# Optimization experiments

Measured on AMD Instinct MI355X. Metric: run time of the kernel, lower is better.

## Reference

```python
import jax, jax.numpy as jnp
import numpy as np

N = 50000; E = 150000
NODE_IN = 16; EDGE_IN = 19; H = 32  # H = max(2*node_in, 32)
LEAK = 0.1; EPS = 1e-5
LAYER_DINS = (16, 32, 32)


def _leaky(x):
    return jnp.where(x >= 0, x, LEAK * x)


def _bn(x, g, b):
    # BatchNorm1d in training mode: batch statistics, biased variance
    m = x.mean(0)
    v = x.var(0)
    return (x - m) * jax.lax.rsqrt(v + EPS) * g + b


def setup_inputs() -> dict:
    key = jax.random.key(0)
    keys = iter(jax.random.split(key, 64))

    def rn(shape, s=0.05):
        return jax.random.normal(next(keys), shape, dtype=jnp.float32) * s

    inp = {
        'x': jax.random.normal(next(keys), (N, NODE_IN), dtype=jnp.float32),
        'edge_index': jax.random.randint(next(keys), (2, E), 0, N),
        'e': jax.random.normal(next(keys), (E, EDGE_IN), dtype=jnp.float32),
        'xbatch': jnp.zeros((N,), dtype=jnp.int32),
        'bn_node_g': jnp.ones((NODE_IN,), jnp.float32), 'bn_node_b': jnp.zeros((NODE_IN,), jnp.float32),
        'bn_edge_g': jnp.ones((EDGE_IN,), jnp.float32), 'bn_edge_b': jnp.zeros((EDGE_IN,), jnp.float32),
    }
    for l, din in enumerate(LAYER_DINS):
        inp[f'l{l}_nnW1'] = rn((EDGE_IN, din));      inp[f'l{l}_nnb1'] = jnp.zeros((din,), jnp.float32)
        inp[f'l{l}_nnW2'] = rn((din, din * H));       inp[f'l{l}_nnb2'] = jnp.zeros((din * H,), jnp.float32)
        inp[f'l{l}_root'] = rn((din, H));             inp[f'l{l}_bias'] = jnp.zeros((H,), jnp.float32)
    # MetaLayer predictor: EdgeModel(H, EDGE_IN, leak) and NodeModel(H, 2, leak)
    inp['em_W1'] = rn((2 * H + EDGE_IN, H)); inp['em_b1'] = jnp.zeros((H,), jnp.float32)
    inp['em_W2'] = rn((H, H));               inp['em_b2'] = jnp.zeros((H,), jnp.float32)
    inp['nm1_W1'] = rn((2 * H, H));          inp['nm1_b1'] = jnp.zeros((H,), jnp.float32)
    inp['nm1_W2'] = rn((H, H));              inp['nm1_b2'] = jnp.zeros((H,), jnp.float32)
    inp['nm2_W1'] = rn((2 * H, H));          inp['nm2_b1'] = jnp.zeros((H,), jnp.float32)
    inp['nm2_W2'] = rn((H, 2));              inp['nm2_b2'] = jnp.zeros((2,), jnp.float32)
    return inp


def _forward(x, e, edge_index, p):
    (bn_node_g, bn_node_b, bn_edge_g, bn_edge_b,
     l0_nnW1, l0_nnb1, l0_nnW2, l0_nnb2, l0_root, l0_bias,
     l1_nnW1, l1_nnb1, l1_nnW2, l1_nnb2, l1_root, l1_bias,
     l2_nnW1, l2_nnb1, l2_nnW2, l2_nnb2, l2_root, l2_bias,
     em_W1, em_b1, em_W2, em_b2,
     nm1_W1, nm1_b1, nm1_W2, nm1_b2,
     nm2_W1, nm2_b1, nm2_W2, nm2_b2) = p

    e = _bn(e, bn_edge_g, bn_edge_b)
    x = _bn(x, bn_node_g, bn_node_b)
    row, col = edge_index[0], edge_index[1]  # source, target (PyG convention)

    layers = [(l0_nnW1, l0_nnb1, l0_nnW2, l0_nnb2, l0_root, l0_bias),
              (l1_nnW1, l1_nnb1, l1_nnW2, l1_nnb2, l1_root, l1_bias),
              (l2_nnW1, l2_nnb1, l2_nnW2, l2_nnb2, l2_root, l2_bias)]
    for (W1, b1, W2, b2, root, bias), din in zip(layers, LAYER_DINS):
        # edge MLP -> per-edge weight matrix [E, din, H]
        w = _leaky(_leaky(e @ W1 + b1) @ W2 + b2).reshape(E, din, H)
        msg = jnp.einsum('ei,eio->eo', x[row], w)              # gather + per-edge matvec
        agg = jax.ops.segment_sum(msg, col, num_segments=N)     # scatter-add ('add' aggr)
        x = agg + x @ root + bias                                # NNConv root weight + bias

    # MetaLayer predictor
    e2 = _leaky(jnp.concatenate([x[row], x[col], e], axis=1) @ em_W1 + em_b1) @ em_W2 + em_b2
    h = _leaky(jnp.concatenate([x[row], e2], axis=1) @ nm1_W1 + nm1_b1) @ nm1_W2 + nm1_b2
    cnt = jnp.clip(jax.ops.segment_sum(jnp.ones((E,), x.dtype), col, num_segments=N), 1.0)
    agg = jax.ops.segment_sum(h, col, num_segments=N) / cnt[:, None]
    xo = _leaky(jnp.concatenate([x, agg], axis=1) @ nm2_W1 + nm2_b1) @ nm2_W2 + nm2_b2
    return jax.nn.log_softmax(xo, axis=1)  # [N, 2] node_pred


def reference(x, edge_index, e, xbatch,
              bn_node_g, bn_node_b, bn_edge_g, bn_edge_b,
              l0_nnW1, l0_nnb1, l0_nnW2, l0_nnb2, l0_root, l0_bias,
              l1_nnW1, l1_nnb1, l1_nnW2, l1_nnb2, l1_root, l1_bias,
              l2_nnW1, l2_nnb1, l2_nnW2, l2_nnb2, l2_root, l2_bias,
              em_W1, em_b1, em_W2, em_b2,
              nm1_W1, nm1_b1, nm1_W2, nm1_b2,
              nm2_W1, nm2_b1, nm2_W2, nm2_b2):
    p = (bn_node_g, bn_node_b, bn_edge_g, bn_edge_b,
         l0_nnW1, l0_nnb1, l0_nnW2, l0_nnb2, l0_root, l0_bias,
         l1_nnW1, l1_nnb1, l1_nnW2, l1_nnb2, l1_root, l1_bias,
         l2_nnW1, l2_nnb1, l2_nnW2, l2_nnb2, l2_root, l2_bias,
         em_W1, em_b1, em_W2, em_b2,
         nm1_W1, nm1_b1, nm1_W2, nm1_b2,
         nm2_W1, nm2_b1, nm2_W2, nm2_b2)
    return _forward(x, e, edge_index, p)
```

## Files before the change

kernel.cpp:

```cpp
#include <hip/hip_runtime.h>
#include <math.h>

constexpr int NN  = 50000;
constexpr int NE  = 150000;
constexpr int NIN = 16;
constexpr int EIN = 19;
constexpr int HD  = 32;
constexpr int NTILES = NE / 16;
constexpr int NBLK_E = 128;
constexpr int NBLK_X = 64;

#define LEAK  0.1f
#define BNEPS 1e-5f

typedef __attribute__((ext_vector_type(8))) short bfrag;
typedef __attribute__((ext_vector_type(4))) float f32x4;
typedef __attribute__((ext_vector_type(2))) float f32x2;
typedef __attribute__((ext_vector_type(4))) int   i32x4;

__device__ __forceinline__ float lky(float v){ return fmaxf(v, LEAK*v); }
__device__ __forceinline__ unsigned f2bf(float f){
  unsigned u = __float_as_uint(f);
  return ((u + 0x7FFFu + ((u >> 16) & 1u)) >> 16);
}
__device__ __forceinline__ void split8(const float* v, i32x4& h4, i32x4& l4){
  unsigned hs[8], ls[8];
  #pragma unroll
  for(int j = 0; j < 8; j++){
    unsigned hh = f2bf(v[j]);
    float hf = __uint_as_float(hh << 16);
    hs[j] = hh; ls[j] = f2bf(v[j] - hf);
  }
  h4[0] = (int)(hs[0] | (hs[1]<<16)); h4[1] = (int)(hs[2] | (hs[3]<<16));
  h4[2] = (int)(hs[4] | (hs[5]<<16)); h4[3] = (int)(hs[6] | (hs[7]<<16));
  l4[0] = (int)(ls[0] | (ls[1]<<16)); l4[1] = (int)(ls[2] | (ls[3]<<16));
  l4[2] = (int)(ls[4] | (ls[5]<<16)); l4[3] = (int)(ls[6] | (ls[7]<<16));
}

__global__ void zero_kernel(float* __restrict__ p, int n){
  int stride = gridDim.x * blockDim.x;
  for(int i = blockIdx.x*blockDim.x + threadIdx.x; i < n; i += stride) p[i] = 0.f;
}

__global__ __launch_bounds__(256) void stats_all_kernel(const float* __restrict__ e,
                                                        const float* __restrict__ x,
                                                        float* __restrict__ partial_e,
                                                        float* __restrict__ partial_x){
  __shared__ float red[4][40];
  const int tid = threadIdx.x, lane = tid & 63, wid = tid >> 6;
  if(blockIdx.x < NBLK_E){
    float s[EIN], q[EIN];
    #pragma unroll
    for(int c = 0; c < EIN; c++){ s[c] = 0.f; q[c] = 0.f; }
    const int gstride = NBLK_E * 256;
    for(int g = blockIdx.x*256 + tid; g < NE/4; g += gstride){
      const f32x4* p = (const f32x4*)(e + (size_t)g * 76);
      #pragma unroll
      for(int m = 0; m < 19; m++){
        f32x4 v = p[m];
        #pragma unroll
        for(int j = 0; j < 4; j++){
          int c = (4*m + j) % 19;
          s[c] += v[j]; q[c] = fmaf(v[j], v[j], q[c]);
        }
      }
    }
    #pragma unroll
    for(int off = 32; off; off >>= 1){
      #pragma unroll
      for(int c = 0; c < EIN; c++){ s[c] += __shfl_xor(s[c], off); q[c] += __shfl_xor(q[c], off); }
    }
    if(lane == 0){
      #pragma unroll
      for(int c = 0; c < EIN; c++){ red[wid][c] = s[c]; red[wid][20 + c] = q[c]; }
    }
    __syncthreads();
    if(tid < 39 && tid != 19)
      partial_e[blockIdx.x*40 + tid] = red[0][tid] + red[1][tid] + red[2][tid] + red[3][tid];
  } else {
    float s[NIN], q[NIN];
    #pragma unroll
    for(int c = 0; c < NIN; c++){ s[c] = 0.f; q[c] = 0.f; }
    const int bid = blockIdx.x - NBLK_E;
    const int gstride = NBLK_X * 256;
    for(int r = bid*256 + tid; r < NN; r += gstride){
      const f32x4* p = (const f32x4*)(x + (size_t)r * NIN);
      #pragma unroll
      for(int m = 0; m < 4; m++){
        f32x4 v = p[m];
        #pragma unroll
        for(int j = 0; j < 4; j++){
          int c = 4*m + j;
          s[c] += v[j]; q[c] = fmaf(v[j], v[j], q[c]);
        }
      }
    }
    #pragma unroll
    for(int off = 32; off; off >>= 1){
      #pragma unroll
      for(int c = 0; c < NIN; c++){ s[c] += __shfl_xor(s[c], off); q[c] += __shfl_xor(q[c], off); }
    }
    if(lane == 0){
      #pragma unroll
      for(int c = 0; c < NIN; c++){ red[wid][c] = s[c]; red[wid][16 + c] = q[c]; }
    }
    __syncthreads();
    if(tid < 32)
      partial_x[bid*32 + tid] = red[0][tid] + red[1][tid] + red[2][tid] + red[3][tid];
  }
}

__global__ __launch_bounds__(1024) void prep_kernel(const float* __restrict__ partial_e,
                                                    const float* __restrict__ partial_x,
                                                    const float* __restrict__ ge, const float* __restrict__ be,
                                                    const float* __restrict__ gx, const float* __restrict__ bx,
                                                    const float* __restrict__ l0W1, const float* __restrict__ l0b1,
                                                    const float* __restrict__ l1W1, const float* __restrict__ l1b1,
                                                    const float* __restrict__ l2W1, const float* __restrict__ l2b1,
                                                    const float* __restrict__ emW1, const float* __restrict__ emb1,
                                                    const float* __restrict__ emW2, const float* __restrict__ emb2,
                                                    const float* __restrict__ nm1W1, const float* __restrict__ nm1b1,
                                                    const float* __restrict__ nm1W2, const float* __restrict__ nm1b2,
                                                    float* __restrict__ ss_g, float* __restrict__ W1f,
                                                    float* __restrict__ b1f, float* __restrict__ biasP,
                                                    short* __restrict__ predpk){
  __shared__ float ss[70];
  __shared__ float emW1f[608];
  __shared__ float emb1f[32];
  __shared__ float predW[7168];
  const int t = threadIdx.x;

  if(t < EIN){
    float s = 0.f, q = 0.f;
    for(int b = 0; b < NBLK_E; b++){ s += partial_e[b*40 + t]; q += partial_e[b*40 + 20 + t]; }
    float m = s / (float)NE;
    float v = q / (float)NE - m*m;
    float sc = ge[t] * rsqrtf(v + BNEPS);
    ss[t] = sc; ss[EIN + t] = be[t] - m*sc;
  } else if(t >= 32 && t < 32 + NIN){
    int c = t - 32;
    float s = 0.f, q = 0.f;
    for(int b = 0; b < NBLK_X; b++){ s += partial_x[b*32 + c]; q += partial_x[b*32 + 16 + c]; }
    float m = s / (float)NN;
    float v = q / (float)NN - m*m;
    float sc = gx[c] * rsqrtf(v + BNEPS);
    ss[2*EIN + c] = sc; ss[2*EIN + NIN + c] = bx[c] - m*sc;
  }
  __syncthreads();
  if(t < 70) ss_g[t] = ss[t];

  if(t < 128){
    int seg = t >> 5, j = t & 31;
    if(seg == 0){
      if(j < NIN){
        float acc = l0b1[j];
        for(int k = 0; k < EIN; k++){
          W1f[0*640 + k*NIN + j] = ss[k] * l0W1[k*NIN + j];
          acc += ss[EIN+k] * l0W1[k*NIN + j];
        }
        b1f[0*32 + j] = acc;
      }
    } else if(seg == 1){
      float acc = l1b1[j];
      for(int k = 0; k < EIN; k++){
        W1f[1*640 + k*HD + j] = ss[k] * l1W1[k*HD + j];
        acc += ss[EIN+k] * l1W1[k*HD + j];
      }
      b1f[1*32 + j] = acc;
    } else if(seg == 2){
      float acc = l2b1[j];
      for(int k = 0; k < EIN; k++){
        W1f[2*640 + k*HD + j] = ss[k] * l2W1[k*HD + j];
        acc += ss[EIN+k] * l2W1[k*HD + j];
      }
      b1f[2*32 + j] = acc;
    } else {
      float acc = emb1[j];
      for(int k = 0; k < EIN; k++){
        emW1f[k*HD + j] = ss[k] * emW1[(2*HD+k)*HD + j];
        acc += ss[EIN+k] * emW1[(2*HD+k)*HD + j];
      }
      emb1f[j] = acc;
    }
  }
  __syncthreads();

  for(int i = t; i < 224*32; i += 1024){
    int k = i >> 5, n = i & 31;
    float v;
    if(k < 64)       v = emW1[k*32 + n];
    else if(k < 83)  v = emW1f[(k-64)*32 + n];
    else if(k < 96)  v = 0.f;
    else if(k < 128) v = emW2[(k-96)*32 + n];
    else if(k < 192) v = nm1W1[(k-128)*32 + n];
    else             v = nm1W2[(k-192)*32 + n];
    predW[i] = v;
  }
  if(t < 128){
    int s = t >> 5, n = t & 31;
    biasP[t] = (s==0) ? emb1f[n] : (s==1) ? emb2[n] : (s==2) ? nm1b1[n] : nm1b2[n];
  }
  __syncthreads();

  for(int idx = t; idx < 14*512; idx += 1024){
    int c = idx >> 9, l = (idx >> 3) & 63, j = idx & 7;
    int kbg = c >> 1, nc = c & 1;
    int k = kbg*32 + 8*(l>>4) + j;
    int n = nc*16 + (l & 15);
    predpk[idx] = (short)f2bf(predW[k*32 + n]);
  }
}

__global__ __launch_bounds__(256) void w2pack_all_kernel(const float* __restrict__ W20,
                                                         const float* __restrict__ W21,
                                                         const float* __restrict__ W22,
                                                         short* __restrict__ w2pk){
  int idx = blockIdx.x*256 + threadIdx.x;
  if(idx >= 81920) return;
  const float* W2; int DIN, base, ci;
  if(idx < 16384){ W2 = W20; DIN = 16; base = 0;     ci = idx; }
  else if(idx < 49152){ W2 = W21; DIN = 32; base = 32768; ci = idx - 16384; }
  else { W2 = W22; DIN = 32; base = 65536; ci = idx - 49152; }
  int c = ci >> 9, l = (ci >> 3) & 63, j = ci & 7;
  int k = 8*(l>>4) + j;
  int n = c*16 + (l & 15);
  float v = (k < DIN) ? W2[(size_t)k*(DIN*HD) + n] : 0.f;
  w2pk[base + ci] = (short)f2bf(v);
}

__global__ __launch_bounds__(256) void rootn_kernel(const float* __restrict__ x,
                                                    const float* __restrict__ ssx,
                                                    const float* __restrict__ root,
                                                    const float* __restrict__ bias,
                                                    float* __restrict__ x_a){
  __shared__ float rs[NIN*HD];
  __shared__ float scs[NIN], shs[NIN], bs[HD];
  const int tid = threadIdx.x;
  for(int i = tid; i < NIN*HD; i += 256) rs[i] = root[i];
  if(tid < NIN){ scs[tid] = ssx[tid]; shs[tid] = ssx[NIN + tid]; }
  else if(tid < NIN + HD) bs[tid - NIN] = bias[tid - NIN];
  __syncthreads();

  int n = blockIdx.x*256 + tid;
  if(n >= NN) return;
  float xb[NIN];
  const f32x4* xp = (const f32x4*)(x + (size_t)n*NIN);
  #pragma unroll
  for(int g = 0; g < 4; g++){
    f32x4 v = xp[g];
    #pragma unroll
    for(int j = 0; j < 4; j++) xb[g*4+j] = fmaf(v[j], scs[g*4+j], shs[g*4+j]);
  }
  f32x4 a0 = *(const f32x4*)&bs[0],  a1 = *(const f32x4*)&bs[4];
  f32x4 a2 = *(const f32x4*)&bs[8],  a3 = *(const f32x4*)&bs[12];
  f32x4 a4 = *(const f32x4*)&bs[16], a5 = *(const f32x4*)&bs[20];
  f32x4 a6 = *(const f32x4*)&bs[24], a7 = *(const f32x4*)&bs[28];
  #pragma unroll
  for(int k = 0; k < NIN; k++){
    float v = xb[k];
    const f32x4* wp = (const f32x4*)&rs[k*HD];
    f32x4 vv = {v,v,v,v};
    a0 = __builtin_elementwise_fma(vv, wp[0], a0);
    a1 = __builtin_elementwise_fma(vv, wp[1], a1);
    a2 = __builtin_elementwise_fma(vv, wp[2], a2);
    a3 = __builtin_elementwise_fma(vv, wp[3], a3);
    a4 = __builtin_elementwise_fma(vv, wp[4], a4);
    a5 = __builtin_elementwise_fma(vv, wp[5], a5);
    a6 = __builtin_elementwise_fma(vv, wp[6], a6);
    a7 = __builtin_elementwise_fma(vv, wp[7], a7);
  }
  f32x4* outp = (f32x4*)(x_a + (size_t)n*HD);
  outp[0]=a0; outp[1]=a1; outp[2]=a2; outp[3]=a3;
  outp[4]=a4; outp[5]=a5; outp[6]=a6; outp[7]=a7;
}

__global__ __launch_bounds__(256) void t1all_kernel(const float* __restrict__ eraw,
                                                    const float* __restrict__ W1f,
                                                    const float* __restrict__ b1f,
                                                    short* __restrict__ T10,
                                                    short* __restrict__ T11,
                                                    short* __restrict__ T12){
  int e = blockIdx.x*256 + threadIdx.x;
  if(e >= NE) return;
  const float* ep = eraw + (size_t)e*EIN;
  float eb[EIN];
  #pragma unroll
  for(int k = 0; k < EIN; k++) eb[k] = ep[k];

  {
    float tv[16];
    #pragma unroll
    for(int j = 0; j < 16; j++) tv[j] = b1f[j];
    #pragma unroll
    for(int k = 0; k < EIN; k++){
      float v = eb[k];
      #pragma unroll
      for(int j = 0; j < 16; j++) tv[j] = fmaf(v, W1f[k*16 + j], tv[j]);
    }
    unsigned pk[8];
    #pragma unroll
    for(int p = 0; p < 8; p++){
      float a = tv[2*p], b = tv[2*p+1];
      pk[p] = f2bf(fmaxf(a, LEAK*a)) | (f2bf(fmaxf(b, LEAK*b)) << 16);
    }
    i32x4* outp = (i32x4*)(T10 + (size_t)e*32);
    i32x4 v0; v0[0]=(int)pk[0]; v0[1]=(int)pk[1]; v0[2]=(int)pk[2]; v0[3]=(int)pk[3];
    i32x4 v1; v1[0]=(int)pk[4]; v1[1]=(int)pk[5]; v1[2]=(int)pk[6]; v1[3]=(int)pk[7];
    i32x4 zz; zz[0]=0; zz[1]=0; zz[2]=0; zz[3]=0;
    outp[0] = v0; outp[1] = v1; outp[2] = zz; outp[3] = zz;
  }
  #pragma unroll
  for(int l = 1; l < 3; l++){
    const float* Wl = W1f + l*640;
    const float* bl = b1f + l*32;
    short* Tl = (l == 1) ? T11 : T12;
    float tv[32];
    #pragma unroll
    for(int j = 0; j < 32; j++) tv[j] = bl[j];
    #pragma unroll
    for(int k = 0; k < EIN; k++){
      float v = eb[k];
      #pragma unroll
      for(int j = 0; j < 32; j++) tv[j] = fmaf(v, Wl[k*32 + j], tv[j]);
    }
    unsigned pk[16];
    #pragma unroll
    for(int p = 0; p < 16; p++){
      float a = tv[2*p], b = tv[2*p+1];
      pk[p] = f2bf(fmaxf(a, LEAK*a)) | (f2bf(fmaxf(b, LEAK*b)) << 16);
    }
    i32x4* outp = (i32x4*)(Tl + (size_t)e*32);
    #pragma unroll
    for(int g = 0; g < 4; g++){
      i32x4 v; v[0]=(int)pk[g*4]; v[1]=(int)pk[g*4+1]; v[2]=(int)pk[g*4+2]; v[3]=(int)pk[g*4+3];
      outp[g] = v;
    }
  }
}

template<int DIN>
__global__ __launch_bounds__(256) void rootv2_kernel(const float* __restrict__ xin,
                                                     const float* __restrict__ root,
                                                     const float* __restrict__ bias,
                                                     float* __restrict__ xout){
  int n = blockIdx.x*256 + threadIdx.x;
  if(n >= NN) return;
  float xr[DIN];
  const f32x4* xp = (const f32x4*)(xin + (size_t)n*DIN);
  #pragma unroll
  for(int g = 0; g < DIN/4; g++){ f32x4 v = xp[g];
    #pragma unroll
    for(int j = 0; j < 4; j++) xr[g*4+j] = v[j]; }
  float acc[HD];
  #pragma unroll
  for(int o = 0; o < HD; o++) acc[o] = bias[o];
  #pragma unroll
  for(int k = 0; k < DIN; k++){
    float v = xr[k];
    #pragma unroll
    for(int o = 0; o < HD; o++) acc[o] = fmaf(v, root[k*HD + o], acc[o]);
  }
  f32x4* outp = (f32x4*)(xout + (size_t)n*HD);
  #pragma unroll
  for(int g = 0; g < 8; g++){ f32x4 v; v[0]=acc[g*4]; v[1]=acc[g*4+1]; v[2]=acc[g*4+2]; v[3]=acc[g*4+3]; outp[g] = v; }
}

template<int DIN, int NCH, int HALVES, int NORM>
__global__ __launch_bounds__(512) void msg7_kernel(const short* __restrict__ T1,
                                                   const int* __restrict__ rowp,
                                                   const int* __restrict__ colp,
                                                   const float* __restrict__ xin,
                                                   const float* __restrict__ ssx,
                                                   const short* __restrict__ w2p,
                                                   const float* __restrict__ b2,
                                                   float* __restrict__ xout){
  constexpr int CH = NCH / HALVES;
  __shared__ short w2s[CH*512];
  __shared__ float b2s[NCH*16];
  __shared__ float xgs[8][DIN][16];

  const int tid = threadIdx.x;
  const int l   = tid & 63;
  const int wid = tid >> 6;
  const int grp = l >> 4, lo16 = l & 15;
  const int tile = blockIdx.x*8 + wid;
  const bool active = tile < NTILES;
  const int e0 = tile * 16;

  if(active){
    int r = rowp[e0 + lo16];
    if(DIN == 32){
      const f32x4* xp = (const f32x4*)(xin + (size_t)r*32 + grp*8);
      f32x4 a = xp[0], b = xp[1];
      #pragma unroll
      for(int j = 0; j < 4; j++) xgs[wid][grp*8 + j][lo16]     = a[j];
      #pragma unroll
      for(int j = 0; j < 4; j++) xgs[wid][grp*8 + 4 + j][lo16] = b[j];
    } else {
      const f32x4* xp = (const f32x4*)(xin + (size_t)r*16 + grp*4);
      f32x4 a = xp[0];
      if(NORM){
        f32x4 sc = *(const f32x4*)(ssx + grp*4);
        f32x4 sh = *(const f32x4*)(ssx + NIN + grp*4);
        a = __builtin_elementwise_fma(a, sc, sh);
      }
      #pragma unroll
      for(int j = 0; j < 4; j++) xgs[wid][grp*4 + j][lo16] = a[j];
    }
  }

  bfrag af = {0,0,0,0,0,0,0,0};
  if(active) af = *(const bfrag*)(T1 + (size_t)(e0 + lo16)*32 + grp*8);

  f32x2 m0a = {0.f,0.f}, m0b = {0.f,0.f}, m1a = {0.f,0.f}, m1b = {0.f,0.f};

  for(int h = 0; h < HALVES; h++){
    if(h) __syncthreads();
    for(int t = tid; t < CH*64; t += 512)
      ((i32x4*)w2s)[t] = ((const i32x4*)w2p)[h*CH*64 + t];
    if(h == 0)
      for(int t = tid; t < NCH*16; t += 512) b2s[t] = b2[t];
    __syncthreads();

    if(active){
      #pragma unroll 4
      for(int i = 0; i < CH/2; i++){
        const int cg = h*CH + 2*i;
        const int ig = cg >> 1;
        float bv0 = b2s[cg*16 + lo16];
        float bv1 = b2s[(cg+1)*16 + lo16];
        f32x4 c0 = {bv0,bv0,bv0,bv0};
        f32x4 c1 = {bv1,bv1,bv1,bv1};
        bfrag b0 = *(const bfrag*)&w2s[((2*i  )*64 + l)*8];
        bfrag b1 = *(const bfrag*)&w2s[((2*i+1)*64 + l)*8];
        f32x4 u0 = __builtin_amdgcn_mfma_f32_16x16x32_bf16(af, b0, c0, 0, 0, 0);
        f32x4 u1 = __builtin_amdgcn_mfma_f32_16x16x32_bf16(af, b1, c1, 0, 0, 0);

        f32x4 xv = *(const f32x4*)&xgs[wid][ig][grp*4];
        f32x2 xva = {xv[0], xv[1]}, xvb = {xv[2], xv[3]};
        f32x2 u0a = {u0[0],u0[1]}, u0b = {u0[2],u0[3]};
        f32x2 u1a = {u1[0],u1[1]}, u1b = {u1[2],u1[3]};
        f32x2 a0a = __builtin_elementwise_max(u0a, u0a*LEAK);
        f32x2 a0b = __builtin_elementwise_max(u0b, u0b*LEAK);
        f32x2 a1a = __builtin_elementwise_max(u1a, u1a*LEAK);
        f32x2 a1b = __builtin_elementwise_max(u1b, u1b*LEAK);
        m0a = __builtin_elementwise_fma(xva, a0a, m0a);
        m0b = __builtin_elementwise_fma(xvb, a0b, m0b);
        m1a = __builtin_elementwise_fma(xva, a1a, m1a);
        m1b = __builtin_elementwise_fma(xvb, a1b, m1b);
      }
    }
  }

  if(active){
    float m0[4] = {m0a[0], m0a[1], m0b[0], m0b[1]};
    float m1[4] = {m1a[0], m1a[1], m1b[0], m1b[1]};
    #pragma unroll
    for(int reg = 0; reg < 4; reg++){
      int ce = colp[e0 + grp*4 + reg];
      atomicAdd(&xout[(size_t)ce*HD + lo16],      m0[reg]);
      atomicAdd(&xout[(size_t)ce*HD + 16 + lo16], m1[reg]);
    }
  }
}

__global__ __launch_bounds__(256, 4) void pred6_kernel(const float* __restrict__ x,
                                                       const float* __restrict__ eraw,
                                                       const int* __restrict__ rowp,
                                                       const int* __restrict__ colp,
                                                       const short* __restrict__ predpk,
                                                       const float* __restrict__ biasP,
                                                       float* __restrict__ agg,
                                                       float* __restrict__ cnt){
  __shared__ short fAhi[4][16][104];
  __shared__ short fAlo[4][16][104];
  __shared__ short uAhi[4][16][40];
  __shared__ short uAlo[4][16][40];

  const int tid = threadIdx.x;
  const int l = tid & 63, wid = tid >> 6;
  const int grp = l >> 4, lo16 = l & 15;

  bfrag wb[14];
  #pragma unroll
  for(int c = 0; c < 14; c++) wb[c] = *(const bfrag*)(predpk + ((size_t)c*64 + l)*8);
  float bP[8];
  #pragma unroll
  for(int s = 0; s < 4; s++){
    bP[s*2]   = biasP[s*32 + lo16];
    bP[s*2+1] = biasP[s*32 + 16 + lo16];
  }

  f32x4 z; z[0]=0.f; z[1]=0.f; z[2]=0.f; z[3]=0.f;
  const int tbase = (blockIdx.x*4 + wid) * 2;

  for(int tt = 0; tt < 2; tt++){
    const int tile = tbase + tt;
    if(tile >= NTILES) break;
    const int e0 = tile * 16;

    {
      float v[8];
      i32x4 h4, l4;
      int r = rowp[e0 + lo16];
      const float* xp = x + (size_t)r*32 + grp*8;
      #pragma unroll
      for(int j = 0; j < 8; j++) v[j] = xp[j];
      split8(v, h4, l4);
      *(i32x4*)&fAhi[wid][lo16][grp*8] = h4;
      *(i32x4*)&fAlo[wid][lo16][grp*8] = l4;

      int c = colp[e0 + lo16];
      const float* xq = x + (size_t)c*32 + grp*8;
      #pragma unroll
      for(int j = 0; j < 8; j++) v[j] = xq[j];
      split8(v, h4, l4);
      *(i32x4*)&fAhi[wid][lo16][32 + grp*8] = h4;
      *(i32x4*)&fAlo[wid][lo16][32 + grp*8] = l4;

      const float* ep = eraw + (size_t)(e0 + lo16)*EIN;
      #pragma unroll
      for(int j = 0; j < 8; j++){ int f = grp*8 + j; v[j] = (f < EIN) ? ep[f] : 0.f; }
      split8(v, h4, l4);
      *(i32x4*)&fAhi[wid][lo16][64 + grp*8] = h4;
      *(i32x4*)&fAlo[wid][lo16][64 + grp*8] = l4;
    }

    #pragma unroll
    for(int nc = 0; nc < 2; nc++){
      f32x4 acc = z;
      #pragma unroll
      for(int kb = 0; kb < 3; kb++){
        bfrag ah = *(const bfrag*)&fAhi[wid][lo16][kb*32 + grp*8];
        bfrag al = *(const bfrag*)&fAlo[wid][lo16][kb*32 + grp*8];
        acc = __builtin_amdgcn_mfma_f32_16x16x32_bf16(ah, wb[kb*2 + nc], acc, 0, 0, 0);
        acc = __builtin_amdgcn_mfma_f32_16x16x32_bf16(al, wb[kb*2 + nc], acc, 0, 0, 0);
      }
      int n = nc*16 + lo16;
      float bv = bP[nc];
      #pragma unroll
      for(int reg = 0; reg < 4; reg++){
        float uv = acc[reg] + bv; uv = fmaxf(uv, LEAK*uv);
        unsigned hh = f2bf(uv);
        float hf = __uint_as_float(hh << 16);
        uAhi[wid][grp*4 + reg][n] = (short)hh;
        uAlo[wid][grp*4 + reg][n] = (short)f2bf(uv - hf);
      }
    }

    #pragma unroll
    for(int nc = 0; nc < 2; nc++){
      f32x4 acc = z;
      bfrag ah = *(const bfrag*)&uAhi[wid][lo16][grp*8];
      bfrag al = *(const bfrag*)&uAlo[wid][lo16][grp*8];
      acc = __builtin_amdgcn_mfma_f32_16x16x32_bf16(ah, wb[6 + nc], acc, 0, 0, 0);
      acc = __builtin_amdgcn_mfma_f32_16x16x32_bf16(al, wb[6 + nc], acc, 0, 0, 0);
      int n = nc*16 + lo16;
      float bv = bP[2 + nc];
      #pragma unroll
      for(int reg = 0; reg < 4; reg++){
        float ev = acc[reg] + bv;
        unsigned hh = f2bf(ev);
        float hf = __uint_as_float(hh << 16);
        fAhi[wid][grp*4 + reg][32 + n] = (short)hh;
        fAlo[wid][grp*4 + reg][32 + n] = (short)f2bf(ev - hf);
      }
    }

    #pragma unroll
    for(int nc = 0; nc < 2; nc++){
      f32x4 acc = z;
      #pragma unroll
      for(int kb = 0; kb < 2; kb++){
        bfrag ah = *(const bfrag*)&fAhi[wid][lo16][kb*32 + grp*8];
        bfrag al = *(const bfrag*)&fAlo[wid][lo16][kb*32 + grp*8];
        acc = __builtin_amdgcn_mfma_f32_16x16x32_bf16(ah, wb[8 + kb*2 + nc], acc, 0, 0, 0);
        acc = __builtin_amdgcn_mfma_f32_16x16x32_bf16(al, wb[8 + kb*2 + nc], acc, 0, 0, 0);
      }
      int n = nc*16 + lo16;
      float bv = bP[4 + nc];
      #pragma unroll
      for(int reg = 0; reg < 4; reg++){
        float vv = acc[reg] + bv; vv = fmaxf(vv, LEAK*vv);
        unsigned hh = f2bf(vv);
        float hf = __uint_as_float(hh << 16);
        uAhi[wid][grp*4 + reg][n] = (short)hh;
        uAlo[wid][grp*4 + reg][n] = (short)f2bf(vv - hf);
      }
    }

    int ce[4];
    #pragma unroll
    for(int reg = 0; reg < 4; reg++) ce[reg] = colp[e0 + grp*4 + reg];

    #pragma unroll
    for(int nc = 0; nc < 2; nc++){
      f32x4 acc = z;
      bfrag ah = *(const bfrag*)&uAhi[wid][lo16][grp*8];
      bfrag al = *(const bfrag*)&uAlo[wid][lo16][grp*8];
      acc = __builtin_amdgcn_mfma_f32_16x16x32_bf16(ah, wb[12 + nc], acc, 0, 0, 0);
      acc = __builtin_amdgcn_mfma_f32_16x16x32_bf16(al, wb[12 + nc], acc, 0, 0, 0);
      int n = nc*16 + lo16;
      float bv = bP[6 + nc];
      #pragma unroll
      for(int reg = 0; reg < 4; reg++)
        atomicAdd(&agg[(size_t)ce[reg]*HD + n], acc[reg] + bv);
    }

    if(l < 16) atomicAdd(&cnt[colp[e0 + l]], 1.f);
  }
}

__global__ __launch_bounds__(256) void final2_kernel(const float* __restrict__ x,
                                                     const float* __restrict__ agg,
                                                     const float* __restrict__ cnt,
                                                     const float* __restrict__ W1,
                                                     const float* __restrict__ b1,
                                                     const float* __restrict__ W2,
                                                     const float* __restrict__ b2,
                                                     float* __restrict__ out){
  __shared__ float w1s[2*HD*HD];
  __shared__ float w2s[HD*2];
  __shared__ float b1s[HD];
  __shared__ float b2s[2];
  const int tid = threadIdx.x;
  for(int i = tid; i < 2*HD*HD; i += 256) w1s[i] = W1[i];
  if(tid < 64) w2s[tid] = W2[tid];
  if(tid < HD) b1s[tid] = b1[tid];
  if(tid < 2)  b2s[tid] = b2[tid];
  __syncthreads();

  int n = blockIdx.x*256 + tid;
  if(n >= NN) return;
  float inv = 1.f / fmaxf(cnt[n], 1.f);

  float xin[HD], ain[HD];
  const f32x4* xp = (const f32x4*)(x + (size_t)n*HD);
  const f32x4* ap = (const f32x4*)(agg + (size_t)n*HD);
  #pragma unroll
  for(int g = 0; g < 8; g++){
    f32x4 v = xp[g];
    #pragma unroll
    for(int j = 0; j < 4; j++) xin[g*4+j] = v[j];
  }
  #pragma unroll
  for(int g = 0; g < 8; g++){
    f32x4 v = ap[g];
    #pragma unroll
    for(int j = 0; j < 4; j++) ain[g*4+j] = v[j] * inv;
  }

  f32x4 a0 = *(const f32x4*)&b1s[0],  a1 = *(const f32x4*)&b1s[4];
  f32x4 a2 = *(const f32x4*)&b1s[8],  a3 = *(const f32x4*)&b1s[12];
  f32x4 a4 = *(const f32x4*)&b1s[16], a5 = *(const f32x4*)&b1s[20];
  f32x4 a6 = *(const f32x4*)&b1s[24], a7 = *(const f32x4*)&b1s[28];
  #pragma unroll
  for(int k = 0; k < HD; k++){
    float v = xin[k];
    const f32x4* wp = (const f32x4*)&w1s[k*HD];
    f32x4 vv = {v,v,v,v};
    a0 = __builtin_elementwise_fma(vv, wp[0], a0);
    a1 = __builtin_elementwise_fma(vv, wp[1], a1);
    a2 = __builtin_elementwise_fma(vv, wp[2], a2);
    a3 = __builtin_elementwise_fma(vv, wp[3], a3);
    a4 = __builtin_elementwise_fma(vv, wp[4], a4);
    a5 = __builtin_elementwise_fma(vv, wp[5], a5);
    a6 = __builtin_elementwise_fma(vv, wp[6], a6);
    a7 = __builtin_elementwise_fma(vv, wp[7], a7);
  }
  #pragma unroll
  for(int k = 0; k < HD; k++){
    float v = ain[k];
    const f32x4* wp = (const f32x4*)&w1s[(HD+k)*HD];
    f32x4 vv = {v,v,v,v};
    a0 = __builtin_elementwise_fma(vv, wp[0], a0);
    a1 = __builtin_elementwise_fma(vv, wp[1], a1);
    a2 = __builtin_elementwise_fma(vv, wp[2], a2);
    a3 = __builtin_elementwise_fma(vv, wp[3], a3);
    a4 = __builtin_elementwise_fma(vv, wp[4], a4);
    a5 = __builtin_elementwise_fma(vv, wp[5], a5);
    a6 = __builtin_elementwise_fma(vv, wp[6], a6);
    a7 = __builtin_elementwise_fma(vv, wp[7], a7);
  }

  float t[HD];
  *(f32x4*)&t[0]  = a0; *(f32x4*)&t[4]  = a1; *(f32x4*)&t[8]  = a2; *(f32x4*)&t[12] = a3;
  *(f32x4*)&t[16] = a4; *(f32x4*)&t[20] = a5; *(f32x4*)&t[24] = a6; *(f32x4*)&t[28] = a7;

  float o0 = b2s[0], o1 = b2s[1];
  #pragma unroll
  for(int k = 0; k < HD; k++){
    float v = lky(t[k]);
    o0 = fmaf(v, w2s[k*2],   o0);
    o1 = fmaf(v, w2s[k*2+1], o1);
  }

  float m  = fmaxf(o0, o1);
  float ls = m + logf(expf(o0 - m) + expf(o1 - m));
  out[(size_t)n*2]   = o0 - ls;
  out[(size_t)n*2+1] = o1 - ls;
}

extern "C" void kernel_launch(void* const* d_in, const int* in_sizes, int n_in,
                              void* d_out, int out_size, void* d_ws, size_t ws_size,
                              hipStream_t stream){
  const float* x  = (const float*)d_in[0];
  const int*   ei = (const int*)  d_in[1];
  const float* e  = (const float*)d_in[2];
  const float* bn_node_g = (const float*)d_in[4];
  const float* bn_node_b = (const float*)d_in[5];
  const float* bn_edge_g = (const float*)d_in[6];
  const float* bn_edge_b = (const float*)d_in[7];
  const float* lW1[3], *lb1[3], *lW2[3], *lb2[3], *lroot[3], *lbias[3];
  for(int l = 0; l < 3; l++){
    lW1[l]   = (const float*)d_in[8 + 6*l + 0];
    lb1[l]   = (const float*)d_in[8 + 6*l + 1];
    lW2[l]   = (const float*)d_in[8 + 6*l + 2];
    lb2[l]   = (const float*)d_in[8 + 6*l + 3];
    lroot[l] = (const float*)d_in[8 + 6*l + 4];
    lbias[l] = (const float*)d_in[8 + 6*l + 5];
  }
  const float* emW1  = (const float*)d_in[26];
  const float* emb1  = (const float*)d_in[27];
  const float* emW2  = (const float*)d_in[28];
  const float* emb2  = (const float*)d_in[29];
  const float* nm1W1 = (const float*)d_in[30];
  const float* nm1b1 = (const float*)d_in[31];
  const float* nm1W2 = (const float*)d_in[32];
  const float* nm1b2 = (const float*)d_in[33];
  const float* nm2W1 = (const float*)d_in[34];
  const float* nm2b1 = (const float*)d_in[35];
  const float* nm2W2 = (const float*)d_in[36];
  const float* nm2b2 = (const float*)d_in[37];

  const int* rowp = ei;
  const int* colp = ei + NE;

  float* ws   = (float*)d_ws;
  float* x_a  = ws;
  float* x_b  = x_a + (size_t)NN*HD;
  float* scr  = x_b + (size_t)NN*HD;
  float* partial_e = scr;
  float* partial_x = scr + 5120;
  float* ss_g      = scr + 7168;
  float* W1f       = scr + 7424;
  float* b1f       = scr + 9344;
  float* biasP     = scr + 9440;
  short* w2pk   = (short*)(scr + 16384);
  short* predpk = w2pk + 3*32768;
  short* T10    = predpk + 8192;
  short* T11    = T10 + (size_t)NE*32;
  short* T12    = T11 + (size_t)NE*32;
  float* agg    = (float*)T10;
  float* cnt    = agg + (size_t)NN*HD;

  stats_all_kernel<<<NBLK_E + NBLK_X, 256, 0, stream>>>(e, x, partial_e, partial_x);
  prep_kernel<<<1, 1024, 0, stream>>>(partial_e, partial_x,
                                      bn_edge_g, bn_edge_b, bn_node_g, bn_node_b,
                                      lW1[0], lb1[0], lW1[1], lb1[1], lW1[2], lb1[2],
                                      emW1, emb1, emW2, emb2,
                                      nm1W1, nm1b1, nm1W2, nm1b2,
                                      ss_g, W1f, b1f, biasP, predpk);
  w2pack_all_kernel<<<320, 256, 0, stream>>>(lW2[0], lW2[1], lW2[2], w2pk);
  t1all_kernel<<<(NE + 255)/256, 256, 0, stream>>>(e, W1f, b1f, T10, T11, T12);

  const int nblocks  = (NN + 255)/256;
  const int m6blocks = (NTILES + 7)/8;

  rootn_kernel<<<nblocks, 256, 0, stream>>>(x, ss_g + 2*EIN, lroot[0], lbias[0], x_a);
  msg7_kernel<NIN, 32, 2, 1><<<m6blocks, 512, 0, stream>>>(T10, rowp, colp, x,
                                                           ss_g + 2*EIN,
                                                           w2pk + 0*32768, lb2[0], x_a);
  rootv2_kernel<HD><<<nblocks, 256, 0, stream>>>(x_a, lroot[1], lbias[1], x_b);
  msg7_kernel<HD, 64, 2, 0><<<m6blocks, 512, 0, stream>>>(T11, rowp, colp, x_a,
                                                          nullptr,
                                                          w2pk + 1*32768, lb2[1], x_b);
  rootv2_kernel<HD><<<nblocks, 256, 0, stream>>>(x_b, lroot[2], lbias[2], x_a);
  msg7_kernel<HD, 64, 2, 0><<<m6blocks, 512, 0, stream>>>(T12, rowp, colp, x_b,
                                                          nullptr,
                                                          w2pk + 2*32768, lb2[2], x_a);

  zero_kernel<<<2048, 256, 0, stream>>>(agg, NN*HD + NN);
  pred6_kernel<<<(NTILES + 7)/8, 256, 0, stream>>>(x_a, e, rowp, colp, predpk, biasP, agg, cnt);
  final2_kernel<<<(NN + 255)/256, 256, 0, stream>>>(x_a, agg, cnt,
                                                    nm2W1, nm2b1, nm2W2, nm2b2,
                                                    (float*)d_out);
}
```

Baseline: 222.6 us.

## Keep W2 fragments in registers and split output halves across wave pairs

```diff
diff --git a/kernel.cpp b/kernel.cpp
--- a/kernel.cpp
+++ b/kernel.cpp
@@ -365,101 +365,86 @@
   for(int g = 0; g < 8; g++){ f32x4 v; v[0]=acc[g*4]; v[1]=acc[g*4+1]; v[2]=acc[g*4+2]; v[3]=acc[g*4+3]; outp[g] = v; }
 }
 
-template<int DIN, int NCH, int HALVES, int NORM>
-__global__ __launch_bounds__(512) void msg7_kernel(const short* __restrict__ T1,
-                                                   const int* __restrict__ rowp,
-                                                   const int* __restrict__ colp,
-                                                   const float* __restrict__ xin,
-                                                   const float* __restrict__ ssx,
-                                                   const short* __restrict__ w2p,
-                                                   const float* __restrict__ b2,
-                                                   float* __restrict__ xout){
-  constexpr int CH = NCH / HALVES;
-  __shared__ short w2s[CH*512];
+template<int DIN, int NCH, int TPW, int NORM>
+__global__ __launch_bounds__(256, 1) void msg8_kernel(const short* __restrict__ T1,
+                                                      const int* __restrict__ rowp,
+                                                      const int* __restrict__ colp,
+                                                      const float* __restrict__ xin,
+                                                      const float* __restrict__ ssx,
+                                                      const short* __restrict__ w2p,
+                                                      const float* __restrict__ b2,
+                                                      float* __restrict__ xout){
+  constexpr int NCHP = NCH / 2;
   __shared__ float b2s[NCH*16];
-  __shared__ float xgs[8][DIN][16];
+  __shared__ float xgs[4][DIN][16];
 
   const int tid = threadIdx.x;
   const int l   = tid & 63;
   const int wid = tid >> 6;
   const int grp = l >> 4, lo16 = l & 15;
-  const int tile = blockIdx.x*8 + wid;
-  const bool active = tile < NTILES;
-  const int e0 = tile * 16;
-
-  if(active){
-    int r = rowp[e0 + lo16];
-    if(DIN == 32){
-      const f32x4* xp = (const f32x4*)(xin + (size_t)r*32 + grp*8);
-      f32x4 a = xp[0], b = xp[1];
-      #pragma unroll
-      for(int j = 0; j < 4; j++) xgs[wid][grp*8 + j][lo16]     = a[j];
-      #pragma unroll
-      for(int j = 0; j < 4; j++) xgs[wid][grp*8 + 4 + j][lo16] = b[j];
-    } else {
-      const f32x4* xp = (const f32x4*)(xin + (size_t)r*16 + grp*4);
-      f32x4 a = xp[0];
-      if(NORM){
-        f32x4 sc = *(const f32x4*)(ssx + grp*4);
-        f32x4 sh = *(const f32x4*)(ssx + NIN + grp*4);
-        a = __builtin_elementwise_fma(a, sc, sh);
-      }
-      #pragma unroll
-      for(int j = 0; j < 4; j++) xgs[wid][grp*4 + j][lo16] = a[j];
-    }
-  }
-
-  bfrag af = {0,0,0,0,0,0,0,0};
-  if(active) af = *(const bfrag*)(T1 + (size_t)(e0 + lo16)*32 + grp*8);
-
-  f32x2 m0a = {0.f,0.f}, m0b = {0.f,0.f}, m1a = {0.f,0.f}, m1b = {0.f,0.f};
-
-  for(int h = 0; h < HALVES; h++){
-    if(h) __syncthreads();
-    for(int t = tid; t < CH*64; t += 512)
-      ((i32x4*)w2s)[t] = ((const i32x4*)w2p)[h*CH*64 + t];
-    if(h == 0)
-      for(int t = tid; t < NCH*16; t += 512) b2s[t] = b2[t];
-    __syncthreads();
-
-    if(active){
-      #pragma unroll 4
-      for(int i = 0; i < CH/2; i++){
-        const int cg = h*CH + 2*i;
-        const int ig = cg >> 1;
-        float bv0 = b2s[cg*16 + lo16];
-        float bv1 = b2s[(cg+1)*16 + lo16];
-        f32x4 c0 = {bv0,bv0,bv0,bv0};
-        f32x4 c1 = {bv1,bv1,bv1,bv1};
-        bfrag b0 = *(const bfrag*)&w2s[((2*i  )*64 + l)*8];
-        bfrag b1 = *(const bfrag*)&w2s[((2*i+1)*64 + l)*8];
-        f32x4 u0 = __builtin_amdgcn_mfma_f32_16x16x32_bf16(af, b0, c0, 0, 0, 0);
-        f32x4 u1 = __builtin_amdgcn_mfma_f32_16x16x32_bf16(af, b1, c1, 0, 0, 0);
-
-        f32x4 xv = *(const f32x4*)&xgs[wid][ig][grp*4];
-        f32x2 xva = {xv[0], xv[1]}, xvb = {xv[2], xv[3]};
-        f32x2 u0a = {u0[0],u0[1]}, u0b = {u0[2],u0[3]};
-        f32x2 u1a = {u1[0],u1[1]}, u1b = {u1[2],u1[3]};
-        f32x2 a0a = __builtin_elementwise_max(u0a, u0a*LEAK);
-        f32x2 a0b = __builtin_elementwise_max(u0b, u0b*LEAK);
-        f32x2 a1a = __builtin_elementwise_max(u1a, u1a*LEAK);
-        f32x2 a1b = __builtin_elementwise_max(u1b, u1b*LEAK);
-        m0a = __builtin_elementwise_fma(xva, a0a, m0a);
-        m0b = __builtin_elementwise_fma(xvb, a0b, m0b);
-        m1a = __builtin_elementwise_fma(xva, a1a, m1a);
-        m1b = __builtin_elementwise_fma(xvb, a1b, m1b);
-      }
-    }
-  }
-
-  if(active){
-    float m0[4] = {m0a[0], m0a[1], m0b[0], m0b[1]};
-    float m1[4] = {m1a[0], m1a[1], m1b[0], m1b[1]};
+  const int pair   = wid >> 1;
+  const int parity = wid & 1;
+
+  for(int t = tid; t < NCH*16; t += 256) b2s[t] = b2[t];
+
+  bfrag wb[NCHP];
+  #pragma unroll
+  for(int i = 0; i < NCHP; i++)
+    wb[i] = *(const bfrag*)(w2p + ((size_t)(2*i + parity)*64 + l)*8);
+  __syncthreads();
+
+  const int tbase = (blockIdx.x*2 + pair) * TPW;
+
+  for(int tt = 0; tt < TPW; tt++){
+    const int tile = tbase + tt;
+    if(tile >= NTILES) break;
+    const int e0 = tile * 16;
+
+    {
+      int r = rowp[e0 + lo16];
+      if(DIN == 32){
+        const f32x4* xp = (const f32x4*)(xin + (size_t)r*32 + grp*8);
+        f32x4 a = xp[0], b = xp[1];
+        #pragma unroll
+        for(int j = 0; j < 4; j++) xgs[wid][grp*8 + j][lo16]     = a[j];
+        #pragma unroll
+        for(int j = 0; j < 4; j++) xgs[wid][grp*8 + 4 + j][lo16] = b[j];
+      } else {
+        const f32x4* xp = (const f32x4*)(xin + (size_t)r*16 + grp*4);
+        f32x4 a = xp[0];
+        if(NORM){
+          f32x4 sc = *(const f32x4*)(ssx + grp*4);
+          f32x4 sh = *(const f32x4*)(ssx + NIN + grp*4);
+          a = __builtin_elementwise_fma(a, sc, sh);
+        }
+        #pragma unroll
+        for(int j = 0; j < 4; j++) xgs[wid][grp*4 + j][lo16] = a[j];
+      }
+    }
+
+    bfrag af = *(const bfrag*)(T1 + (size_t)(e0 + lo16)*32 + grp*8);
+
+    f32x2 ma = {0.f, 0.f}, mb = {0.f, 0.f};
+
+    #pragma unroll
+    for(int i = 0; i < NCHP; i++){
+      float bv = b2s[(2*i + parity)*16 + lo16];
+      f32x4 c = {bv, bv, bv, bv};
+      f32x4 u = __builtin_amdgcn_mfma_f32_16x16x32_bf16(af, wb[i], c, 0, 0, 0);
+      f32x4 xv = *(const f32x4*)&xgs[wid][i][grp*4];
+      f32x2 xva = {xv[0], xv[1]}, xvb = {xv[2], xv[3]};
+      f32x2 ua = {u[0], u[1]}, ub = {u[2], u[3]};
+      f32x2 la = __builtin_elementwise_max(ua, ua*LEAK);
+      f32x2 lb = __builtin_elementwise_max(ub, ub*LEAK);
+      ma = __builtin_elementwise_fma(xva, la, ma);
+      mb = __builtin_elementwise_fma(xvb, lb, mb);
+    }
+
+    float m[4] = {ma[0], ma[1], mb[0], mb[1]};
     #pragma unroll
     for(int reg = 0; reg < 4; reg++){
       int ce = colp[e0 + grp*4 + reg];
-      atomicAdd(&xout[(size_t)ce*HD + lo16],      m0[reg]);
-      atomicAdd(&xout[(size_t)ce*HD + 16 + lo16], m1[reg]);
+      atomicAdd(&xout[(size_t)ce*HD + parity*16 + lo16], m[reg]);
     }
   }
 }
@@ -765,18 +750,18 @@
   t1all_kernel<<<(NE + 255)/256, 256, 0, stream>>>(e, W1f, b1f, T10, T11, T12);
 
   const int nblocks  = (NN + 255)/256;
-  const int m6blocks = (NTILES + 7)/8;
+  const int m8blocks = (NTILES + 3)/4;
 
   rootn_kernel<<<nblocks, 256, 0, stream>>>(x, ss_g + 2*EIN, lroot[0], lbias[0], x_a);
-  msg7_kernel<NIN, 32, 2, 1><<<m6blocks, 512, 0, stream>>>(T10, rowp, colp, x,
+  msg8_kernel<NIN, 32, 2, 1><<<m8blocks, 256, 0, stream>>>(T10, rowp, colp, x,
                                                            ss_g + 2*EIN,
                                                            w2pk + 0*32768, lb2[0], x_a);
   rootv2_kernel<HD><<<nblocks, 256, 0, stream>>>(x_a, lroot[1], lbias[1], x_b);
-  msg7_kernel<HD, 64, 2, 0><<<m6blocks, 512, 0, stream>>>(T11, rowp, colp, x_a,
+  msg8_kernel<HD, 64, 2, 0><<<m8blocks, 256, 0, stream>>>(T11, rowp, colp, x_a,
                                                           nullptr,
                                                           w2pk + 1*32768, lb2[1], x_b);
   rootv2_kernel<HD><<<nblocks, 256, 0, stream>>>(x_b, lroot[2], lbias[2], x_a);
-  msg7_kernel<HD, 64, 2, 0><<<m6blocks, 512, 0, stream>>>(T12, rowp, colp, x_b,
+  msg8_kernel<HD, 64, 2, 0><<<m8blocks, 256, 0, stream>>>(T12, rowp, colp, x_b,
                                                           nullptr,
                                                           w2pk + 2*32768, lb2[2], x_a);
 
```

Result: slower. 243.0 us (+9.1%).
